# Performance work log

Measured on AMD Instinct MI355X. Metric: run time of the kernel, lower is better.

## Reference

```python
import jax, jax.numpy as jnp
import numpy as np

N_NODES = 50000      # nodes per side (12500 tetrahedra x 4 nodes)
N_GRAPHS = 12500     # graph pairs in the batch
HID = 256


def _tet_edges(n_graphs):
    # 12 directed edges among the 4 nodes of each tetrahedron
    pat = np.array([(a, b) for a in range(4) for b in range(4) if a != b], dtype=np.int64)  # [12,2]
    base = np.arange(n_graphs, dtype=np.int64)[:, None, None] * 4  # [G,1,1]
    ei = (base + pat[None]).reshape(-1, 2).T  # [2, 12*G]
    return jnp.asarray(ei)


def setup_inputs() -> dict:
    key = jax.random.key(0)
    ks = jax.random.split(key, 20)

    def w(k, shape, fan_in):
        return (jax.random.normal(k, shape, dtype=jnp.float32) / np.sqrt(fan_in)).astype(jnp.float32)

    x_1 = jax.random.normal(ks[0], (N_NODES, 3), dtype=jnp.float32)
    x_2 = jax.random.normal(ks[1], (N_NODES, 3), dtype=jnp.float32)
    edge_index_1 = _tet_edges(N_GRAPHS)
    edge_index_2 = _tet_edges(N_GRAPHS)
    batch_1 = jnp.repeat(jnp.arange(N_GRAPHS, dtype=jnp.int64), 4)
    batch_2 = batch_1

    params = dict(
        W1=w(ks[2], (3, HID), 3), b1=jnp.zeros((HID,), jnp.float32),
        W2=w(ks[3], (HID, HID), HID), b2=jnp.zeros((HID,), jnp.float32),
        W3=w(ks[4], (HID, HID), HID), b3=jnp.zeros((HID,), jnp.float32),
        Wl1=w(ks[5], (512, 512), 512), bl1=jnp.zeros((512,), jnp.float32),
        Wl2=w(ks[6], (512, 256), 512), bl2=jnp.zeros((256,), jnp.float32),
        Wl3=w(ks[7], (256, 128), 256), bl3=jnp.zeros((128,), jnp.float32),
        Wl4=w(ks[8], (128, 64), 128), bl4=jnp.zeros((64,), jnp.float32),
    )
    return dict(x_1=x_1, edge_index_1=edge_index_1, batch_1=batch_1,
                x_2=x_2, edge_index_2=edge_index_2, batch_2=batch_2, **params)


def gcn_conv(x, edge_index, W, b):
    # PyG GCNConv: add self loops, symmetric deg normalization, sum aggregate, then bias
    n = x.shape[0]
    loops = jnp.arange(n, dtype=edge_index.dtype)
    src = jnp.concatenate([edge_index[0], loops])
    dst = jnp.concatenate([edge_index[1], loops])
    deg = jax.ops.segment_sum(jnp.ones_like(dst, dtype=x.dtype), dst, num_segments=n)
    dis = jnp.where(deg > 0, jax.lax.rsqrt(jnp.maximum(deg, 1.0)), 0.0)
    norm = dis[src] * dis[dst]                       # [E+N]
    xw = x @ W                                       # [N, out]
    out = jax.ops.segment_sum(norm[:, None] * xw[src], dst, num_segments=n)
    return out + b


def encode(x, edge_index, batch, W1, b1, W2, b2, W3, b3):
    x = jax.nn.relu(gcn_conv(x, edge_index, W1, b1))
    x = jax.nn.relu(gcn_conv(x, edge_index, W2, b2))
    x = jax.nn.relu(gcn_conv(x, edge_index, W3, b3))
    # global_mean_pool
    s = jax.ops.segment_sum(x, batch, num_segments=N_GRAPHS)
    cnt = jax.ops.segment_sum(jnp.ones((x.shape[0],), x.dtype), batch, num_segments=N_GRAPHS)
    return s / jnp.maximum(cnt, 1.0)[:, None]


def reference(x_1, edge_index_1, batch_1, x_2, edge_index_2, batch_2,
              W1, b1, W2, b2, W3, b3,
              Wl1, bl1, Wl2, bl2, Wl3, bl3, Wl4, bl4):
    h1 = encode(x_1, edge_index_1, batch_1, W1, b1, W2, b2, W3, b3)
    h2 = encode(x_2, edge_index_2, batch_2, W1, b1, W2, b2, W3, b3)
    h = jnp.concatenate([h1, h2], axis=1)            # [G, 512]
    h = jax.nn.relu(h @ Wl1 + bl1)
    h = jax.nn.relu(h @ Wl2 + bl2)
    h = jax.nn.relu(h @ Wl3 + bl3)
    h = h @ Wl4 + bl4                                # layer_4: no relu (as in source)
    return jax.nn.sigmoid(h)                         # [G, 64]
```

## Files before the change

### kernel.cpp

```cpp
#include <hip/hip_runtime.h>


typedef _Float16 half8 __attribute__((ext_vector_type(8)));
typedef float floatx4 __attribute__((ext_vector_type(4)));

struct PrepArgsV12 { const float* in[6]; };

__global__ __launch_bounds__(256) void v12_prep(PrepArgsV12 p, _Float16* Bf) {
  const int sz[6]  = {65536, 65536, 262144, 131072, 32768, 8192};
  const int lgN[6] = {8, 8, 9, 8, 7, 6};
  const int off[6] = {0, 65536, 131072, 393216, 524288, 557056};
  int e = blockIdx.x * 256 + threadIdx.x;
  for (int i = 0; i < 6; ++i) {
    if (e < sz[i]) {
      int N = 1 << lgN[i];
      int k = e >> lgN[i];
      int n = e & (N - 1);
      float w = p.in[i][e];
      int kb = k >> 5, quad = (k >> 3) & 3, j = k & 7;
      int nt = n >> 4;
      int lane = quad * 16 + (n & 15);
      int dst = ((kb * (N >> 4) + nt) * 64 + lane) * 8 + j;
      Bf[off[i] + dst] = (_Float16)w;
      return;
    }
    e -= sz[i];
  }
}

template<int MT, int NT, int TNT, int KB, bool ENC_IN, int OUT_MODE>
__device__ __forceinline__ void layer(
    const _Float16* __restrict__ Bf, const float* __restrict__ bias,
    _Float16* sA, float* __restrict__ outg, int pair0, int nw, int m0, int lane) {
  const int quad = lane >> 4, lr = lane & 15;
  const int n0 = nw * (NT * 16);
  const int STRIDE = ENC_IN ? 264 : 520;
  const _Float16* bp = Bf + ((size_t)(nw * NT) * 64 + lane) * 8;

  floatx4 acc[MT][NT];
#pragma unroll
  for (int mt = 0; mt < MT; ++mt)
#pragma unroll
    for (int nt = 0; nt < NT; ++nt)
      acc[mt][nt] = (floatx4){0.f, 0.f, 0.f, 0.f};

  half8 bbuf[3][NT];
#pragma unroll
  for (int nt = 0; nt < NT; ++nt) {
    bbuf[0][nt] = *(const half8*)(bp + nt * 512);
    bbuf[1][nt] = *(const half8*)(bp + (size_t)TNT * 512 + nt * 512);
  }

#pragma unroll
  for (int kb = 0; kb < KB; ++kb) {
    const int cur = kb % 3;
    half8 av[MT];
#pragma unroll
    for (int mt = 0; mt < MT; ++mt)
      av[mt] = *(const half8*)(sA + (m0 + mt * 16 + lr) * STRIDE + kb * 32 + quad * 8);
#pragma unroll
    for (int nt = 0; nt < NT; ++nt)
#pragma unroll
      for (int mt = 0; mt < MT; ++mt)
        acc[mt][nt] = __builtin_amdgcn_mfma_f32_16x16x32_f16(av[mt], bbuf[cur][nt], acc[mt][nt], 0, 0, 0);
    if (kb + 2 < KB) {
      const int nxt = (kb + 2) % 3;
#pragma unroll
      for (int nt = 0; nt < NT; ++nt)
        bbuf[nxt][nt] = *(const half8*)(bp + (size_t)(kb + 2) * (TNT * 512) + nt * 512);
    }
  }

  __syncthreads();

#pragma unroll
  for (int nt = 0; nt < NT; ++nt) {
    int c = n0 + nt * 16 + lr;
    float bv = bias[c];
#pragma unroll
    for (int mt = 0; mt < MT; ++mt) {
#pragma unroll
      for (int reg = 0; reg < 4; ++reg) {
        int r = m0 + mt * 16 + quad * 4 + reg;
        float v = acc[mt][nt][reg] + bv;
        if (OUT_MODE <= 2) {
          v = fmaxf(v, 0.f);
          int a;
          if (OUT_MODE == 0)      a = r * 264 + c;
          else if (OUT_MODE == 1) a = (r >> 1) * 520 + (r & 1) * 256 + c;
          else                    a = r * 520 + c;
          sA[a] = (_Float16)v;
        } else {
          if (r < 50) outg[(size_t)(pair0 + r) * 64 + c] = 1.0f / (1.0f + expf(-v));
        }
      }
    }
  }
  __syncthreads();
}

__global__ __launch_bounds__(512, 2) void v12_mega(
    const float* __restrict__ x1, const float* __restrict__ x2,
    const float* __restrict__ W1, const float* __restrict__ b1,
    const _Float16* __restrict__ Bf,
    const float* __restrict__ b2, const float* __restrict__ b3,
    const float* __restrict__ bl1, const float* __restrict__ bl2,
    const float* __restrict__ bl3, const float* __restrict__ bl4,
    float* __restrict__ outg) {
  __shared__ _Float16 sA[33280];
  __shared__ float sM[112][3];

  int tid = threadIdx.x;
  int wave = tid >> 6, lane = tid & 63;
  int pair0 = blockIdx.x * 50;

  for (int i = tid; i < 16640; i += 512) ((float*)sA)[i] = 0.f;

  if (tid < 112) {
    int r = tid;
    float a0 = 0.f, a1 = 0.f, a2 = 0.f;
    if (r < 100) {
      int g = pair0 + (r >> 1);
      const float* q = ((r & 1) ? x2 : x1) + (size_t)g * 12;
      a0 = 0.25f * (q[0] + q[3] + q[6] + q[9]);
      a1 = 0.25f * (q[1] + q[4] + q[7] + q[10]);
      a2 = 0.25f * (q[2] + q[5] + q[8] + q[11]);
    }
    sM[r][0] = a0; sM[r][1] = a1; sM[r][2] = a2;
  }
  __syncthreads();

  {
    int c = tid & 255;
    float w0 = W1[c], w1 = W1[256 + c], w2 = W1[512 + c], bb = b1[c];
    for (int r = (tid >> 8); r < 112; r += 2) {
      float v = fmaxf(sM[r][0] * w0 + sM[r][1] * w1 + sM[r][2] * w2 + bb, 0.f);
      sA[r * 264 + c] = (_Float16)v;
    }
  }
  __syncthreads();

  layer<7, 2, 16,  8, true,  0>(Bf + 0,      b2,  sA, nullptr, pair0, wave, 0, lane);
  layer<7, 2, 16,  8, true,  1>(Bf + 65536,  b3,  sA, nullptr, pair0, wave, 0, lane);
  layer<4, 4, 32, 16, false, 2>(Bf + 131072, bl1, sA, nullptr, pair0, wave, 0, lane);
  layer<4, 2, 16, 16, false, 2>(Bf + 393216, bl2, sA, nullptr, pair0, wave, 0, lane);
  layer<4, 1,  8,  8, false, 2>(Bf + 524288, bl3, sA, nullptr, pair0, wave, 0, lane);
  layer<2, 1,  4,  4, false, 3>(Bf + 557056, bl4, sA, outg,    pair0,
                                wave & 3, (wave >> 2) * 32, lane);
}

extern "C" void kernel_launch(void* const* d_in, const int* in_sizes, int n_in,
                              void* d_out, int out_size, void* d_ws, size_t ws_size,
                              hipStream_t stream) {
  const float* x1  = (const float*)d_in[0];
  const float* x2  = (const float*)d_in[3];
  const float* W1  = (const float*)d_in[6];
  const float* b1  = (const float*)d_in[7];
  const float* W2  = (const float*)d_in[8];
  const float* b2  = (const float*)d_in[9];
  const float* W3  = (const float*)d_in[10];
  const float* b3  = (const float*)d_in[11];
  const float* Wl1 = (const float*)d_in[12];
  const float* bl1 = (const float*)d_in[13];
  const float* Wl2 = (const float*)d_in[14];
  const float* bl2 = (const float*)d_in[15];
  const float* Wl3 = (const float*)d_in[16];
  const float* bl3 = (const float*)d_in[17];
  const float* Wl4 = (const float*)d_in[18];
  const float* bl4 = (const float*)d_in[19];

  _Float16* Bf = (_Float16*)d_ws;

  PrepArgsV12 pa;
  pa.in[0] = W2;  pa.in[1] = W3;  pa.in[2] = Wl1;
  pa.in[3] = Wl2; pa.in[4] = Wl3; pa.in[5] = Wl4;

  v12_prep<<<dim3(2208), dim3(256), 0, stream>>>(pa, Bf);
  v12_mega<<<dim3(250), dim3(512), 0, stream>>>(x1, x2, W1, b1, Bf,
                                                b2, b3, bl1, bl2, bl3, bl4,
                                                (float*)d_out);
}
```

Measured before the change: 122.3 us.

## Use 1024-thread blocks with finer per-wave N split and fragment-wise weight prep

The mega kernel now launches 16 waves per block instead of 8. Each wave owns fewer N tiles, and the last two layers get new M/N splits across the waves. The prep kernel gives each thread a whole 8-element fp16 fragment and writes it with one vector store, cutting the prep grid from 2208 to 276 blocks. The goal is more waves to hide latency within each block and fewer prep threads. In exchange, each wave reuses its A operand across fewer N tiles, and only one 1024-thread block is likely resident per CU, where two 512-thread blocks fit before.

New measurement: 121.3 us. Within noise of the previous version (-0.8%).

```diff
diff --git a/kernel.cpp b/kernel.cpp
--- a/kernel.cpp
+++ b/kernel.cpp
@@ -4,27 +4,29 @@
 typedef _Float16 half8 __attribute__((ext_vector_type(8)));
 typedef float floatx4 __attribute__((ext_vector_type(4)));
 
-struct PrepArgsV12 { const float* in[6]; };
+struct PrepArgsV13 { const float* in[6]; };
 
-__global__ __launch_bounds__(256) void v12_prep(PrepArgsV12 p, _Float16* Bf) {
-  const int sz[6]  = {65536, 65536, 262144, 131072, 32768, 8192};
-  const int lgN[6] = {8, 8, 9, 8, 7, 6};
-  const int off[6] = {0, 65536, 131072, 393216, 524288, 557056};
-  int e = blockIdx.x * 256 + threadIdx.x;
+__global__ __launch_bounds__(256) void v13_prep(PrepArgsV13 p, _Float16* Bf) {
+  const int frags[6] = {8192, 8192, 32768, 16384, 4096, 1024};
+  const int lgN[6]   = {8, 8, 9, 8, 7, 6};
+  const int off[6]   = {0, 65536, 131072, 393216, 524288, 557056};
+  int f = blockIdx.x * 256 + threadIdx.x;
   for (int i = 0; i < 6; ++i) {
-    if (e < sz[i]) {
+    if (f < frags[i]) {
       int N = 1 << lgN[i];
-      int k = e >> lgN[i];
-      int n = e & (N - 1);
-      float w = p.in[i][e];
-      int kb = k >> 5, quad = (k >> 3) & 3, j = k & 7;
-      int nt = n >> 4;
-      int lane = quad * 16 + (n & 15);
-      int dst = ((kb * (N >> 4) + nt) * 64 + lane) * 8 + j;
-      Bf[off[i] + dst] = (_Float16)w;
+      int lane = f & 63, rem = f >> 6;
+      int nt = rem & ((N >> 4) - 1);
+      int kb = rem >> (lgN[i] - 4);
+      int n = nt * 16 + (lane & 15);
+      int k0 = kb * 32 + (lane >> 4) * 8;
+      const float* src = p.in[i] + (size_t)k0 * N + n;
+      half8 v;
+#pragma unroll
+      for (int j = 0; j < 8; ++j) v[j] = (_Float16)src[(size_t)j * N];
+      *(half8*)(Bf + off[i] + (size_t)f * 8) = v;
       return;
     }
-    e -= sz[i];
+    f -= frags[i];
   }
 }
 
@@ -99,7 +101,7 @@
   __syncthreads();
 }
 
-__global__ __launch_bounds__(512, 2) void v12_mega(
+__global__ __launch_bounds__(1024) void v13_mega(
     const float* __restrict__ x1, const float* __restrict__ x2,
     const float* __restrict__ W1, const float* __restrict__ b1,
     const _Float16* __restrict__ Bf,
@@ -114,7 +116,7 @@
   int wave = tid >> 6, lane = tid & 63;
   int pair0 = blockIdx.x * 50;
 
-  for (int i = tid; i < 16640; i += 512) ((float*)sA)[i] = 0.f;
+  for (int i = tid; i < 16640; i += 1024) ((float*)sA)[i] = 0.f;
 
   if (tid < 112) {
     int r = tid;
@@ -133,20 +135,21 @@
   {
     int c = tid & 255;
     float w0 = W1[c], w1 = W1[256 + c], w2 = W1[512 + c], bb = b1[c];
-    for (int r = (tid >> 8); r < 112; r += 2) {
+    for (int r = (tid >> 8); r < 112; r += 4) {
       float v = fmaxf(sM[r][0] * w0 + sM[r][1] * w1 + sM[r][2] * w2 + bb, 0.f);
       sA[r * 264 + c] = (_Float16)v;
     }
   }
   __syncthreads();
 
-  layer<7, 2, 16,  8, true,  0>(Bf + 0,      b2,  sA, nullptr, pair0, wave, 0, lane);
-  layer<7, 2, 16,  8, true,  1>(Bf + 65536,  b3,  sA, nullptr, pair0, wave, 0, lane);
-  layer<4, 4, 32, 16, false, 2>(Bf + 131072, bl1, sA, nullptr, pair0, wave, 0, lane);
-  layer<4, 2, 16, 16, false, 2>(Bf + 393216, bl2, sA, nullptr, pair0, wave, 0, lane);
-  layer<4, 1,  8,  8, false, 2>(Bf + 524288, bl3, sA, nullptr, pair0, wave, 0, lane);
-  layer<2, 1,  4,  4, false, 3>(Bf + 557056, bl4, sA, outg,    pair0,
-                                wave & 3, (wave >> 2) * 32, lane);
+  layer<7, 1, 16,  8, true,  0>(Bf + 0,      b2,  sA, nullptr, pair0, wave, 0, lane);
+  layer<7, 1, 16,  8, true,  1>(Bf + 65536,  b3,  sA, nullptr, pair0, wave, 0, lane);
+  layer<4, 2, 32, 16, false, 2>(Bf + 131072, bl1, sA, nullptr, pair0, wave, 0, lane);
+  layer<4, 1, 16, 16, false, 2>(Bf + 393216, bl2, sA, nullptr, pair0, wave, 0, lane);
+  layer<2, 1,  8,  8, false, 2>(Bf + 524288, bl3, sA, nullptr, pair0,
+                                wave & 7, (wave >> 3) * 32, lane);
+  layer<1, 1,  4,  4, false, 3>(Bf + 557056, bl4, sA, outg,    pair0,
+                                wave & 3, (wave >> 2) * 16, lane);
 }
 
 extern "C" void kernel_launch(void* const* d_in, const int* in_sizes, int n_in,
@@ -171,12 +174,12 @@
 
   _Float16* Bf = (_Float16*)d_ws;
 
-  PrepArgsV12 pa;
+  PrepArgsV13 pa;
   pa.in[0] = W2;  pa.in[1] = W3;  pa.in[2] = Wl1;
   pa.in[3] = Wl2; pa.in[4] = Wl3; pa.in[5] = Wl4;
 
-  v12_prep<<<dim3(2208), dim3(256), 0, stream>>>(pa, Bf);
-  v12_mega<<<dim3(250), dim3(512), 0, stream>>>(x1, x2, W1, b1, Bf,
-                                                b2, b3, bl1, bl2, bl3, bl4,
-                                                (float*)d_out);
+  v13_prep<<<dim3(276), dim3(256), 0, stream>>>(pa, Bf);
+  v13_mega<<<dim3(250), dim3(1024), 0, stream>>>(x1, x2, W1, b1, Bf,
+                                                 b2, b3, bl1, bl2, bl3, bl4,
+                                                 (float*)d_out);
 }
```
